# Performance work log

Measured on AMD Instinct MI355X. Metric: run time of the kernel, lower is better.

## Reference

```python
import jax, jax.numpy as jnp
import numpy as np

S, B, C = 56, 32, 1024
T = 48
H = 1024          # hidden_size_decoder (== context_size C)
EMB = 512
RANK = 128
VOCAB = 32000


def setup_inputs() -> dict:
    key = jax.random.key(0)
    ks = jax.random.split(key, 16)
    w = 0.05
    inp = {
        "encoded": jax.random.normal(ks[0], (S, B, C), jnp.float32),
        "encoder_state": jax.random.normal(ks[1], (2, B, H), jnp.float32) * 0.1,
        "tgt_tokens": jax.random.randint(ks[2], (B, T), 0, VOCAB),
        "enc_lens": jax.random.randint(ks[3], (B,), S // 2, S + 1).astype(jnp.int32),
        "tgt_lens": jax.random.randint(ks[4], (B,), T // 2, T + 1).astype(jnp.int32),
        "E": jax.random.normal(ks[5], (VOCAB, RANK), jnp.float32) * w,
        "P": jax.random.normal(ks[6], (RANK, EMB), jnp.float32) * w,
        "W0": jax.random.normal(ks[7], (EMB + C, 4 * H), jnp.float32) * w,
        "U0": jax.random.normal(ks[8], (H, 4 * H), jnp.float32) * w,
        "b0": jnp.zeros((4 * H,), jnp.float32),
        "W1": jax.random.normal(ks[9], (H, 4 * H), jnp.float32) * w,
        "U1": jax.random.normal(ks[10], (H, 4 * H), jnp.float32) * w,
        "b1": jnp.zeros((4 * H,), jnp.float32),
        "Wo": jax.random.normal(ks[11], (H + C, EMB), jnp.float32) * w,
        "bo": jnp.zeros((EMB,), jnp.float32),
    }
    return inp


def _lstm_cell(x, h, c, W, U, b):
    gates = x @ W + h @ U + b                      # [B, 4H]
    i, f, g, o = jnp.split(gates, 4, axis=-1)      # torch LSTMCell gate order
    c_new = jax.nn.sigmoid(f) * c + jax.nn.sigmoid(i) * jnp.tanh(g)
    h_new = jax.nn.sigmoid(o) * jnp.tanh(c_new)
    return h_new, c_new


def reference(encoded, encoder_state, tgt_tokens, enc_lens, tgt_lens,
              E, P, W0, U0, b0, W1, U1, b1, Wo, bo):
    # encoded: [S, B, C] (padded encoder outputs), encoder_state: [L=2, B, H]
    enc_b = jnp.transpose(encoded, (1, 0, 2))                 # [B, S, C]
    enc_mask = jnp.arange(S)[None, :] >= enc_lens[:, None]    # [B, S] True = pad

    # factorized embedding lookup (dropout p=0)
    emb = (E[tgt_tokens] @ P)                                 # [B, T, EMB]
    emb_t = jnp.transpose(emb, (1, 0, 2))[: T - 1]            # [T-1, B, EMB]

    h0 = encoder_state                                        # [2, B, H]
    c0 = jnp.zeros_like(encoder_state)
    ctx0 = jnp.zeros((B, C), encoded.dtype)

    def step(carry, x_emb):
        h, c, ctx = carry
        x = jnp.concatenate([x_emb, ctx], axis=-1)            # [B, EMB+C]
        h0n, c0n = _lstm_cell(x, h[0], c[0], W0, U0, b0)
        h1n, c1n = _lstm_cell(h0n, h[1], c[1], W1, U1, b1)
        query = h1n                                           # no context projection
        scores = jnp.einsum("bsc,bc->bs", enc_b, query)       # [B, S]
        scores = jnp.where(enc_mask, -jnp.inf, scores)
        p_att = jax.nn.softmax(scores, axis=-1)
        ctx_new = jnp.einsum("bs,bsc->bc", p_att, enc_b)      # [B, C]
        return (jnp.stack([h0n, h1n]), jnp.stack([c0n, c1n]), ctx_new), (h1n, ctx_new)

    _, (decs, ctxs) = jax.lax.scan(step, (h0, c0, ctx0), emb_t)  # each [T-1, B, *]

    feats = jnp.concatenate([decs, ctxs], axis=-1)            # [T-1, B, H+C]
    hproj = jnp.tanh(feats @ Wo + bo)                          # [T-1, B, EMB]
    logits = (hproj @ P.T) @ E.T                               # [T-1, B, VOCAB]

    labels = tgt_tokens[:, 1:].T                               # [T-1, B]
    logp = jax.nn.log_softmax(logits, axis=-1)
    nll = -jnp.take_along_axis(logp, labels[..., None], axis=-1)[..., 0]
    valid = jnp.arange(T - 1)[:, None] < (tgt_lens[None, :] - 1)  # step t predicts token t+1
    loss = jnp.sum(jnp.where(valid, nll, 0.0))                 # CrossEntropyLoss(reduction='sum')
    return loss
```

## Files before the change

### kernel.cpp

```cpp
#include <hip/hip_runtime.h>
#include <math.h>

#define S_   56
#define B_   32
#define C_   1024
#define T_   48
#define TS   47
#define H_   1024
#define EMB_ 512
#define RANK_ 128
#define VOCAB_ 32000
#define G4   4096
#define NBLK 256

#define FL_DONE 8192
#define FL_P    8224
#define FL_SIZE 10496

using bf16x8 = __attribute__((ext_vector_type(8))) __bf16;
using f32x4  = __attribute__((ext_vector_type(4))) float;

__device__ __forceinline__ float sigmoidf_(float x){ return 1.0f/(1.0f+expf(-x)); }
__device__ __forceinline__ float b2f(__bf16 x){ return (float)x; }
__device__ __forceinline__ f32x4 z4(){ f32x4 z = {0.f,0.f,0.f,0.f}; return z; }

#define AG __HIP_MEMORY_SCOPE_AGENT
__device__ __forceinline__ void stc_u64(void* p, unsigned long long v){
  __hip_atomic_store((unsigned long long*)p, v, __ATOMIC_RELAXED, AG);
}

struct RedShared {
  float red[4][2][16][18];
};
struct AttnShared {
  union { float hS[1024]; float cred[7][64][8]; } u;
  float sS[64];
  float pS[64];
};
union alignas(16) SharedU { RedShared r; AttnShared a; };

__device__ __forceinline__ void bar_arrive(unsigned* bars, int bi, unsigned e){
  asm volatile("s_waitcnt vmcnt(0)" ::: "memory");
  __syncthreads();
  if (threadIdx.x == 0)
    __hip_atomic_store(bars + (size_t)bi*32, e, __ATOMIC_RELAXED, AG);
}
__device__ __forceinline__ void bar_wait_all(unsigned* bars, int bi, unsigned e){
  if (bi == 255){
    if (threadIdx.x < 256){
      while (__hip_atomic_load(bars + (size_t)threadIdx.x*32, __ATOMIC_RELAXED, AG) < e) {}
    }
    __syncthreads();
    if (threadIdx.x == 0)
      __hip_atomic_store(bars + FL_DONE, e, __ATOMIC_RELAXED, AG);
  } else {
    if (threadIdx.x == 0){
      while (__hip_atomic_load(bars + FL_DONE, __ATOMIC_RELAXED, AG) < e) {}
    }
    __syncthreads();
  }
  asm volatile("" ::: "memory");
}
__device__ __forceinline__ void bar_wait_direct(unsigned* bars, unsigned e){
  if (threadIdx.x < 256){
    while (__hip_atomic_load(bars + (size_t)threadIdx.x*32, __ATOMIC_RELAXED, AG) < e) {}
  }
  __syncthreads();
  asm volatile("" ::: "memory");
}
__device__ __forceinline__ void pflag_wait(unsigned* bars, unsigned t){
  if (threadIdx.x < 64){
    while (__hip_atomic_load(bars + FL_P + (size_t)threadIdx.x*32, __ATOMIC_RELAXED, AG) < t)
      __builtin_amdgcn_s_sleep(2);
  }
  __syncthreads();
  asm volatile("" ::: "memory");
}

__global__ void k_init(const float* __restrict__ es, __bf16* h0bm1, __bf16* fm1,
                       unsigned* bars){
  int i = blockIdx.x*blockDim.x + threadIdx.x;
  if (i < 32*H_){
    int b = i >> 10, j = i & 1023;
    h0bm1[(size_t)b*1024 + j]       = (__bf16)es[i];
    fm1[(size_t)b*2048 + j]         = (__bf16)es[32*H_ + i];
    fm1[(size_t)b*2048 + 1024 + j]  = (__bf16)0.0f;
  }
  if (i < FL_SIZE) bars[i] = 0u;
}

__global__ void k_cvt(const float* __restrict__ src, __bf16* __restrict__ dst, int n){
  int i = (blockIdx.x*blockDim.x + threadIdx.x)*4;
  if (i < n){
    float4 v = *(const float4*)(src + i);
    dst[i+0]=(__bf16)v.x; dst[i+1]=(__bf16)v.y; dst[i+2]=(__bf16)v.z; dst[i+3]=(__bf16)v.w;
  }
}

__global__ void k_embed(const float* __restrict__ E, const float* __restrict__ P,
                        const int* __restrict__ tok, __bf16* __restrict__ embb){
  int blk = blockIdx.x;
  int t = blk >> 5, b = blk & 31, tid = threadIdx.x;
  __shared__ float er[RANK_];
  int tk = tok[b*T_ + t];
  er[tid] = E[(size_t)tk*RANK_ + tid];
  __syncthreads();
  float4 acc = {0.f,0.f,0.f,0.f};
  int e = tid*4;
  for (int r2 = 0; r2 < RANK_; r2++){
    float ev = er[r2];
    float4 p = *(const float4*)(P + (size_t)r2*EMB_ + e);
    acc.x += ev*p.x; acc.y += ev*p.y; acc.z += ev*p.z; acc.w += ev*p.w;
  }
  size_t o = (size_t)blk*EMB_ + e;
  embb[o+0]=(__bf16)acc.x; embb[o+1]=(__bf16)acc.y;
  embb[o+2]=(__bf16)acc.z; embb[o+3]=(__bf16)acc.w;
}

__global__ void k_pack2(const float* __restrict__ W, int K1, const float* __restrict__ U,
                        __bf16* __restrict__ dst, int NCH){
  int ch = blockIdx.x;
  int g  = blockIdx.y >> 2;
  int band = blockIdx.y & 3;
  int tid = threadIdx.x;
  __shared__ __bf16 Tl[32][264];
  {
    int r = tid>>3, cs = tid&7;
    int kk = ch*32 + r;
    const float* src = (kk < K1) ? (W + (size_t)kk*G4 + g*1024 + band*256 + cs*32)
                                 : (U + (size_t)(kk-K1)*G4 + g*1024 + band*256 + cs*32);
    #pragma unroll
    for (int u=0;u<8;u++){
      float4 v = *(const float4*)(src + u*4);
      Tl[r][cs*32+u*4+0]=(__bf16)v.x; Tl[r][cs*32+u*4+1]=(__bf16)v.y;
      Tl[r][cs*32+u*4+2]=(__bf16)v.z; Tl[r][cs*32+u*4+3]=(__bf16)v.w;
    }
  }
  __syncthreads();
  int bil = tid>>2, aq = tid&3;
  int bi = band*64 + bil;
  #pragma unroll
  for (int q=0;q<4;q++){
    __bf16 o8[8];
    #pragma unroll
    for (int i=0;i<8;i++) o8[i] = Tl[aq*8+i][bil*4+q];
    int lane = aq*16 + g*4 + q;
    *(bf16x8*)(dst + (((size_t)bi*NCH + ch)*64 + lane)*8) = *(bf16x8*)o8;
  }
}

__global__ void k_packB(const float* __restrict__ src, __bf16* __restrict__ dst,
                        int K, int N, int tr){
  int kk0 = blockIdx.x*32, j0 = blockIdx.y*16, lane = threadIdx.x;
  int am = lane&15, aq = lane>>4;
  int j = j0 + am;
  __bf16 o8[8];
  #pragma unroll
  for (int i=0;i<8;i++){
    int k = kk0 + aq*8 + i;
    float v = tr ? src[(size_t)j*K + k] : src[(size_t)k*N + j];
    o8[i] = (__bf16)v;
  }
  int NCH = K/32, jt = j0>>4, ch = kk0>>5;
  *(bf16x8*)(dst + (((size_t)jt*NCH + ch)*64 + lane)*8) = *(bf16x8*)o8;
}

template<int NC>
__device__ __forceinline__ void accum(f32x4& acc0, f32x4& acc1,
    const __bf16* __restrict__ abase, int rs, const __bf16* wlds,
    int ch0, int am, int aq, int lane)
{
  const __bf16* a0p = abase + (size_t)am*rs + aq*8;
  const __bf16* a1p = abase + (size_t)(am+16)*rs + aq*8;
  const __bf16* wl  = wlds + (size_t)lane*8;
  #pragma unroll
  for (int c=0;c<NC;c++){
    int ch = ch0 + c;
    bf16x8 a0 = *(const bf16x8*)(a0p + (size_t)ch*32);
    bf16x8 a1 = *(const bf16x8*)(a1p + (size_t)ch*32);
    bf16x8 w  = *(const bf16x8*)(wl  + (size_t)ch*512);
    acc0 = __builtin_amdgcn_mfma_f32_16x16x32_bf16(a0, w, acc0, 0, 0, 0);
    acc1 = __builtin_amdgcn_mfma_f32_16x16x32_bf16(a1, w, acc1, 0, 0, 0);
  }
}

__device__ __forceinline__ void reduce_cell(SharedU& su, const f32x4& acc0, const f32x4& acc1,
    int bi, int tid, const float* __restrict__ bias, float& creg,
    __bf16* __restrict__ hout, int stride)
{
  int kw = tid>>6, lane = tid&63, am = lane&15, aq = lane>>4;
  if (kw >= 4){
    #pragma unroll
    for (int rg=0;rg<4;rg++){
      su.r.red[kw-4][0][aq*4+rg][am] = acc0[rg];
      su.r.red[kw-4][1][aq*4+rg][am] = acc1[rg];
    }
  }
  __syncthreads();
  if (kw < 4){
    #pragma unroll
    for (int rg=0;rg<4;rg++){
      su.r.red[kw][0][aq*4+rg][am] += acc0[rg];
      su.r.red[kw][1][aq*4+rg][am] += acc1[rg];
    }
  }
  __syncthreads();
  if (tid < 128){
    int b = tid>>2, q = tid&3;
    int mt = b>>4, r = b&15;
    float G0=0.f, G1=0.f, G2=0.f, G3=0.f;
    #pragma unroll
    for (int w2=0; w2<4; w2++){
      G0 += su.r.red[w2][mt][r][q];
      G1 += su.r.red[w2][mt][r][4+q];
      G2 += su.r.red[w2][mt][r][8+q];
      G3 += su.r.red[w2][mt][r][12+q];
    }
    int j = bi*4 + q;
    float gi = G0 + bias[j];
    float gf = G1 + bias[1024 + j];
    float gg = G2 + bias[2048 + j];
    float go = G3 + bias[3072 + j];
    float ii = sigmoidf_(gi), ff = sigmoidf_(gf), gv = tanhf(gg), oo = sigmoidf_(go);
    float cv = ff*creg + ii*gv;
    float hv = oo*tanhf(cv);
    creg = cv;
    union { __bf16 h; unsigned short s; } hu; hu.h = (__bf16)hv;
    unsigned h0v = hu.s;
    unsigned h1v = __shfl_down(h0v, 1);
    unsigned h2v = __shfl_down(h0v, 2);
    unsigned h3v = __shfl_down(h0v, 3);
    if (q == 0){
      unsigned long long pk = (unsigned long long)(h0v & 0xffffu)
                            | ((unsigned long long)(h1v & 0xffffu) << 16)
                            | ((unsigned long long)(h2v & 0xffffu) << 32)
                            | ((unsigned long long)(h3v & 0xffffu) << 48);
      stc_u64(hout + (size_t)b*stride + bi*4, pk);
    }
  }
}

__device__ __forceinline__ void attn_block(AttnShared& sa, int b, int chalf, int tid,
    const __bf16* __restrict__ encb, const int* __restrict__ enc_lens,
    __bf16* __restrict__ fbt)
{
  if (tid < 128){
    bf16x8 h8 = *(const bf16x8*)(fbt + (size_t)b*2048 + tid*8);
    #pragma unroll
    for (int u=0;u<8;u++) sa.u.hS[tid*8+u] = b2f(h8[u]);
  }
  __syncthreads();
  int w = tid >> 6, lane = tid & 63;
  for (int s = w; s < S_; s += 8){
    const __bf16* er = encb + ((size_t)s*32 + b)*C_;
    float a = 0.f;
    #pragma unroll
    for (int half = 0; half < 2; half++){
      int k = lane*8 + half*512;
      bf16x8 e8 = *(const bf16x8*)(er + k);
      #pragma unroll
      for (int u=0;u<8;u++) a += b2f(e8[u]) * sa.u.hS[k+u];
    }
    #pragma unroll
    for (int off=32; off>0; off>>=1) a += __shfl_down(a, off);
    if (lane == 0) sa.sS[s] = a;
  }
  __syncthreads();
  if (tid < 64){
    int len = enc_lens[b];
    float sc = (tid < len && tid < S_) ? sa.sS[tid] : -1e30f;
    float m = sc;
    #pragma unroll
    for (int off=32; off>0; off>>=1) m = fmaxf(m, __shfl_xor(m, off));
    float e = expf(sc - m);
    float ssum = e;
    #pragma unroll
    for (int off=32; off>0; off>>=1) ssum += __shfl_xor(ssum, off);
    sa.pS[tid] = e / ssum;
  }
  __syncthreads();
  int cg = tid & 63, sg = tid >> 6;
  float a8[8];
  #pragma unroll
  for (int i=0;i<8;i++) a8[i] = 0.f;
  for (int s = sg; s < S_; s += 8){
    float p = sa.pS[s];
    bf16x8 e8 = *(const bf16x8*)(encb + ((size_t)s*32 + b)*C_ + chalf*512 + cg*8);
    #pragma unroll
    for (int i=0;i<8;i++) a8[i] += p * b2f(e8[i]);
  }
  if (sg > 0){
    #pragma unroll
    for (int i=0;i<8;i++) sa.u.cred[sg-1][cg][i] = a8[i];
  }
  __syncthreads();
  if (sg == 0){
    union { __bf16 bb[8]; unsigned long long u[2]; } cu;
    #pragma unroll
    for (int i=0;i<8;i++){
      float v = a8[i];
      #pragma unroll
      for (int k=0;k<7;k++) v += sa.u.cred[k][cg][i];
      cu.bb[i] = (__bf16)v;
    }
    stc_u64(fbt + (size_t)b*2048 + 1024 + chalf*512 + cg*8,     cu.u[0]);
    stc_u64(fbt + (size_t)b*2048 + 1024 + chalf*512 + cg*8 + 4, cu.u[1]);
  }
}

__global__ __launch_bounds__(512) void k_loop(
    const __bf16* __restrict__ WP0, const __bf16* __restrict__ WP1,
    const float* __restrict__ b0, const float* __restrict__ b1,
    __bf16* __restrict__ h0b,
    __bf16* __restrict__ featsb,
    const __bf16* __restrict__ embb,
    const __bf16* __restrict__ encb, const int* __restrict__ enc_lens,
    unsigned* bars)
{
  __shared__ __bf16 wB0[80*512];
  __shared__ __bf16 wB1[64*512];
  __shared__ SharedU su;
  int bi = blockIdx.x, tid = threadIdx.x;
  int kw = tid>>6, lane = tid&63, am = lane&15, aq = lane>>4;

  {
    const bf16x8* g0 = (const bf16x8*)(WP0 + (size_t)bi*80*512);
    const bf16x8* g1 = (const bf16x8*)(WP1 + (size_t)bi*64*512);
    bf16x8* l0 = (bf16x8*)wB0;
    bf16x8* l1 = (bf16x8*)wB1;
    for (int idx = tid; idx < 80*64; idx += 512) l0[idx] = g0[idx];
    for (int idx = tid; idx < 64*64; idx += 512) l1[idx] = g1[idx];
  }
  __syncthreads();

  float c0r = 0.f, c1r = 0.f;
  f32x4 g00 = z4(), g01 = z4(), g10 = z4(), g11 = z4();

  accum<2>(g00, g01, embb,                 512,  wB0, kw*2,    am, aq, lane);
  accum<4>(g00, g01, h0b - 32768 - 1536,   1024, wB0, 48+kw*4, am, aq, lane);

  unsigned e = 0;
  for (int t = 0; t < TS; t++){
    const __bf16* fprev = featsb + ((size_t)(t-1))*65536;
    __bf16* h0t = h0b + (size_t)t*32768;
    __bf16* ft  = featsb + (size_t)t*65536;

    pflag_wait(bars, (unsigned)t);
    accum<4>(g00, g01, fprev + 512, 2048, wB0, 16+kw*4, am, aq, lane);
    reduce_cell(su, g00, g01, bi, tid, b0, c0r, h0t, 1024);
    g00 = z4(); g01 = z4();
    bar_arrive(bars, bi, ++e);
    accum<4>(g10, g11, fprev - 1024, 2048, wB1, 32+kw*4, am, aq, lane);
    bar_wait_all(bars, bi, e);

    accum<4>(g10, g11, h0t, 1024, wB1, kw*4, am, aq, lane);
    reduce_cell(su, g10, g11, bi, tid, b1, c1r, ft, 2048);
    g10 = z4(); g11 = z4();
    bar_arrive(bars, bi, ++e);
    if (t + 1 < TS){
      accum<2>(g00, g01, embb + (size_t)(t+1)*16384, 512,  wB0, kw*2,    am, aq, lane);
      accum<4>(g00, g01, h0t - 1536,                 1024, wB0, 48+kw*4, am, aq, lane);
    }

    if (bi < 64){
      bar_wait_direct(bars, e);
      attn_block(su.a, bi & 31, bi >> 5, tid, encb, enc_lens, ft);
      asm volatile("s_waitcnt vmcnt(0)" ::: "memory");
      __syncthreads();
      if (tid == 0)
        __hip_atomic_store(bars + FL_P + (size_t)bi*32, (unsigned)(t+1), __ATOMIC_RELAXED, AG);
    }
  }
}

__global__ __launch_bounds__(256) void k_hproj_mfma(
    const __bf16* __restrict__ fb, const __bf16* __restrict__ WoP,
    const float* __restrict__ bo, __bf16* __restrict__ hpb)
{
  int nt = blockIdx.x, jb = blockIdx.y, tid = threadIdx.x;
  int w = tid>>6, lane = tid&63;
  int mt = w&1, jw = w>>1;
  int am = lane&15, aq = lane>>4;
  const __bf16* aRow = fb + ((size_t)(nt*32 + mt*16 + am))*2048 + aq*8;
  int jt = jb*2 + jw;
  const __bf16* bptr = WoP + ((size_t)jt*64)*512 + lane*8;
  f32x4 acc = {0,0,0,0};
  bf16x8 ar0 = *(const bf16x8*)(aRow);
  bf16x8 br0 = *(const bf16x8*)(bptr);
  bf16x8 ar1 = *(const bf16x8*)(aRow + 32);
  bf16x8 br1 = *(const bf16x8*)(bptr + 512);
  for (int ch = 0; ch < 64; ch += 2){
    bf16x8 a0 = ar0, b0 = br0, a1 = ar1, b1 = br1;
    if (ch + 2 < 64){
      ar0 = *(const bf16x8*)(aRow + (ch+2)*32);
      br0 = *(const bf16x8*)(bptr + (size_t)(ch+2)*512);
      ar1 = *(const bf16x8*)(aRow + (ch+3)*32);
      br1 = *(const bf16x8*)(bptr + (size_t)(ch+3)*512);
    }
    acc = __builtin_amdgcn_mfma_f32_16x16x32_bf16(a0, b0, acc, 0, 0, 0);
    acc = __builtin_amdgcn_mfma_f32_16x16x32_bf16(a1, b1, acc, 0, 0, 0);
  }
  int jcol = jb*32 + jw*16 + am;
  float bv = bo[jcol];
  #pragma unroll
  for (int rg=0; rg<4; rg++){
    int m = nt*32 + mt*16 + aq*4 + rg;
    hpb[(size_t)m*512 + jcol] = (__bf16)tanhf(acc[rg] + bv);
  }
}

__global__ __launch_bounds__(256) void k_rproj_mfma(
    const __bf16* __restrict__ hpb, const __bf16* __restrict__ PP,
    __bf16* __restrict__ rb)
{
  int nt = blockIdx.x, jb = blockIdx.y, tid = threadIdx.x;
  int w = tid>>6, lane = tid&63;
  int mt = w&1, jw = w>>1;
  int am = lane&15, aq = lane>>4;
  const __bf16* aRow = hpb + ((size_t)(nt*32 + mt*16 + am))*512 + aq*8;
  int jt = jb*2 + jw;
  const __bf16* bptr = PP + ((size_t)jt*16)*512 + lane*8;
  f32x4 acc = {0,0,0,0};
  #pragma unroll
  for (int ch = 0; ch < 16; ch++){
    bf16x8 a = *(const bf16x8*)(aRow + ch*32);
    bf16x8 b = *(const bf16x8*)(bptr + (size_t)ch*512);
    acc = __builtin_amdgcn_mfma_f32_16x16x32_bf16(a, b, acc, 0, 0, 0);
  }
  int jcol = jb*32 + jw*16 + am;
  #pragma unroll
  for (int rg=0; rg<4; rg++){
    int m = nt*32 + mt*16 + aq*4 + rg;
    rb[(size_t)m*RANK_ + jcol] = (__bf16)acc[rg];
  }
}

__global__ __launch_bounds__(256) void k_vocab2(
    const __bf16* __restrict__ rb, const __bf16* __restrict__ Eb,
    const int* __restrict__ tok,
    float* __restrict__ mpart, float* __restrict__ lpart,
    float* __restrict__ lablog)
{
  int vc = blockIdx.x, tid = threadIdx.x;
  int w = tid>>6, lane = tid&63;
  int am = lane&15, aq = lane>>4;
  int vb = vc*128 + w*32;
  bf16x8 bfr[2][4];
  #pragma unroll
  for (int vt=0; vt<2; vt++)
    #pragma unroll
    for (int ks=0; ks<4; ks++)
      bfr[vt][ks] = *(const bf16x8*)(Eb + ((size_t)(vb + vt*16 + am))*RANK_ + ks*32 + aq*8);

  __shared__ float redM[4][32], redL[4][32];
  for (int nt = 0; nt < TS; nt++){
    f32x4 acc[2][2] = {{{0,0,0,0},{0,0,0,0}},{{0,0,0,0},{0,0,0,0}}};
    #pragma unroll
    for (int mt=0; mt<2; mt++){
      #pragma unroll
      for (int ks=0; ks<4; ks++){
        bf16x8 a = *(const bf16x8*)(rb + ((size_t)(nt*32 + mt*16 + am))*RANK_ + ks*32 + aq*8);
        acc[mt][0] = __builtin_amdgcn_mfma_f32_16x16x32_bf16(a, bfr[0][ks], acc[mt][0], 0,0,0);
        acc[mt][1] = __builtin_amdgcn_mfma_f32_16x16x32_bf16(a, bfr[1][ks], acc[mt][1], 0,0,0);
      }
    }
    #pragma unroll
    for (int mt=0; mt<2; mt++){
      #pragma unroll
      for (int rg=0; rg<4; rg++){
        int row = mt*16 + aq*4 + rg;
        int n = nt*32 + row;
        int lbl = tok[row*T_ + nt + 1];
        float v0 = acc[mt][0][rg], v1 = acc[mt][1][rg];
        if (vb + am == lbl)      lablog[n] = v0;
        if (vb + 16 + am == lbl) lablog[n] = v1;
        float m = fmaxf(v0, v1);
        #pragma unroll
        for (int off=1; off<16; off<<=1) m = fmaxf(m, __shfl_xor(m, off));
        float l = expf(v0 - m) + expf(v1 - m);
        #pragma unroll
        for (int off=1; off<16; off<<=1) l += __shfl_xor(l, off);
        if (am == 0){ redM[w][row] = m; redL[w][row] = l; }
      }
    }
    __syncthreads();
    if (tid < 32){
      float M = fmaxf(fmaxf(redM[0][tid], redM[1][tid]), fmaxf(redM[2][tid], redM[3][tid]));
      float L = 0.f;
      #pragma unroll
      for (int ww=0; ww<4; ww++) L += redL[ww][tid]*expf(redM[ww][tid] - M);
      mpart[(size_t)(nt*32 + tid)*250 + vc] = M;
      lpart[(size_t)(nt*32 + tid)*250 + vc] = L;
    }
    __syncthreads();
  }
}

__global__ void k_loss1(const float* __restrict__ mpart, const float* __restrict__ lpart,
                        const float* __restrict__ lablog, const int* __restrict__ tgt_lens,
                        float* __restrict__ tpart){
  int t = blockIdx.x, tid = threadIdx.x;
  int row = tid >> 3, cq = tid & 7;
  int n = t*32 + row;
  float m = -1e30f;
  for (int c = cq; c < 250; c += 8) m = fmaxf(m, mpart[(size_t)n*250 + c]);
  #pragma unroll
  for (int off=1; off<8; off<<=1) m = fmaxf(m, __shfl_xor(m, off));
  float l = 0.f;
  for (int c = cq; c < 250; c += 8) l += lpart[(size_t)n*250 + c]*expf(mpart[(size_t)n*250 + c] - m);
  #pragma unroll
  for (int off=1; off<8; off<<=1) l += __shfl_xor(l, off);
  __shared__ float red[32];
  if (cq == 0)
    red[row] = (t < tgt_lens[row] - 1) ? (m + logf(l) - lablog[n]) : 0.f;
  __syncthreads();
  if (tid == 0){
    float s = 0.f;
    #pragma unroll
    for (int i=0;i<32;i++) s += red[i];
    tpart[t] = s;
  }
}

__global__ void k_loss2(const float* __restrict__ tpart, float* __restrict__ out){
  int tid = threadIdx.x;
  float v = (tid < TS) ? tpart[tid] : 0.f;
  #pragma unroll
  for (int off=32; off>0; off>>=1) v += __shfl_down(v, off);
  if (tid == 0) out[0] = v;
}

extern "C" void kernel_launch(void* const* d_in, const int* in_sizes, int n_in,
                              void* d_out, int out_size, void* d_ws, size_t ws_size,
                              hipStream_t stream){
  const float* enc      = (const float*)d_in[0];
  const float* es       = (const float*)d_in[1];
  const int*   tok      = (const int*)  d_in[2];
  const int*   enc_lens = (const int*)  d_in[3];
  const int*   tgt_lens = (const int*)  d_in[4];
  const float* E        = (const float*)d_in[5];
  const float* P        = (const float*)d_in[6];
  const float* W0       = (const float*)d_in[7];
  const float* U0       = (const float*)d_in[8];
  const float* b0       = (const float*)d_in[9];
  const float* W1       = (const float*)d_in[10];
  const float* U1       = (const float*)d_in[11];
  const float* b1       = (const float*)d_in[12];
  const float* Wo       = (const float*)d_in[13];
  const float* bo       = (const float*)d_in[14];
  float* out = (float*)d_out;

  float* fb = (float*)d_ws;
  size_t fo = 0;
  float* mpart = fb + fo; fo += (size_t)TS*32*250;
  float* lpart = fb + fo; fo += (size_t)TS*32*250;
  float* lab   = fb + fo; fo += (size_t)TS*32;
  float* tpart = fb + fo; fo += 64;
  unsigned* bars = (unsigned*)(fb + fo); fo += FL_SIZE;
  __bf16* bb = (__bf16*)(fb + fo);
  size_t bo2 = 0;
  __bf16* WP0    = bb + bo2; bo2 += (size_t)4096*2560;
  __bf16* WP1    = bb + bo2; bo2 += (size_t)4096*2048;
  __bf16* encb   = bb + bo2; bo2 += (size_t)S_*32*C_;
  __bf16* embb   = bb + bo2; bo2 += (size_t)TS*32*EMB_;
  __bf16* rbuf   = bb + bo2; bo2 += (size_t)TS*32*RANK_;
  __bf16* WoP    = bb + bo2; bo2 += (size_t)2048*512;
  __bf16* PP     = bb + bo2; bo2 += (size_t)512*128;
  __bf16* featsb0= bb + bo2; bo2 += (size_t)(TS+1)*32*2048;
  __bf16* hpb    = bb + bo2; bo2 += (size_t)TS*32*EMB_;
  __bf16* h0b0   = bb + bo2; bo2 += (size_t)(TS+1)*32*1024;
  __bf16* Eb     = WP0;

  __bf16* featsb = featsb0 + (size_t)32*2048;
  __bf16* h0b    = h0b0 + (size_t)32*1024;

  k_init<<<128, 256, 0, stream>>>(es, h0b0, featsb0, bars);
  k_cvt<<<(S_*32*C_/4 + 255)/256, 256, 0, stream>>>(enc, encb, S_*32*C_);
  k_embed<<<TS*32, 128, 0, stream>>>(E, P, tok, embb);
  k_pack2<<<dim3(80,16), 256, 0, stream>>>(W0, 1536, U0, WP0, 80);
  k_pack2<<<dim3(64,16), 256, 0, stream>>>(W1, 1024, U1, WP1, 64);
  k_packB<<<dim3(64,32), 64, 0, stream>>>(Wo, WoP, 2048, 512, 0);
  k_packB<<<dim3(16,8), 64, 0, stream>>>(P, PP, 512, 128, 1);

  k_loop<<<NBLK, 512, 0, stream>>>(WP0, WP1, b0, b1, h0b, featsb,
                                   embb, encb, enc_lens, bars);

  k_cvt<<<(VOCAB_*RANK_/4 + 255)/256, 256, 0, stream>>>(E, Eb, VOCAB_*RANK_);

  k_hproj_mfma<<<dim3(TS,16), 256, 0, stream>>>(featsb, WoP, bo, hpb);
  k_rproj_mfma<<<dim3(TS,4), 256, 0, stream>>>(hpb, PP, rbuf);
  k_vocab2<<<250, 256, 0, stream>>>(rbuf, Eb, tok, mpart, lpart, lab);
  k_loss1<<<TS, 256, 0, stream>>>(mpart, lpart, lab, tgt_lens, tpart);
  k_loss2<<<1, 64, 0, stream>>>(tpart, out);
}
```

Baseline: 1.392 ms.

## Pack LSTM weights inside persistent loop, merge prep kernels, flatten grid barrier

The separate weight-packing kernels and their global bf16 staging buffers are removed. Each persistent block now loads its fp32 W/U columns directly and converts and scatters them into shared memory itself. The encoder conversion is merged into the init kernel, and the E conversion moves ahead of the loop so Eb gets its own buffer. The two-level barrier through a single done-flag is replaced by every block polling all 256 arrival flags with a short sleep, and the attention flag wait sleeps less. This saves launches and a global round trip but adds strided fp32 loads at loop start and more polling traffic on the barrier.

```diff
diff --git a/kernel.cpp b/kernel.cpp
--- a/kernel.cpp
+++ b/kernel.cpp
@@ -13,7 +13,6 @@
 #define G4   4096
 #define NBLK 256
 
-#define FL_DONE 8192
 #define FL_P    8224
 #define FL_SIZE 10496
 
@@ -45,25 +44,10 @@
   if (threadIdx.x == 0)
     __hip_atomic_store(bars + (size_t)bi*32, e, __ATOMIC_RELAXED, AG);
 }
-__device__ __forceinline__ void bar_wait_all(unsigned* bars, int bi, unsigned e){
-  if (bi == 255){
-    if (threadIdx.x < 256){
-      while (__hip_atomic_load(bars + (size_t)threadIdx.x*32, __ATOMIC_RELAXED, AG) < e) {}
-    }
-    __syncthreads();
-    if (threadIdx.x == 0)
-      __hip_atomic_store(bars + FL_DONE, e, __ATOMIC_RELAXED, AG);
-  } else {
-    if (threadIdx.x == 0){
-      while (__hip_atomic_load(bars + FL_DONE, __ATOMIC_RELAXED, AG) < e) {}
-    }
-    __syncthreads();
-  }
-  asm volatile("" ::: "memory");
-}
-__device__ __forceinline__ void bar_wait_direct(unsigned* bars, unsigned e){
+__device__ __forceinline__ void bar_wait(unsigned* bars, unsigned e){
   if (threadIdx.x < 256){
-    while (__hip_atomic_load(bars + (size_t)threadIdx.x*32, __ATOMIC_RELAXED, AG) < e) {}
+    while (__hip_atomic_load(bars + (size_t)threadIdx.x*32, __ATOMIC_RELAXED, AG) < e)
+      __builtin_amdgcn_s_sleep(1);
   }
   __syncthreads();
   asm volatile("" ::: "memory");
@@ -71,15 +55,22 @@
 __device__ __forceinline__ void pflag_wait(unsigned* bars, unsigned t){
   if (threadIdx.x < 64){
     while (__hip_atomic_load(bars + FL_P + (size_t)threadIdx.x*32, __ATOMIC_RELAXED, AG) < t)
-      __builtin_amdgcn_s_sleep(2);
+      __builtin_amdgcn_s_sleep(1);
   }
   __syncthreads();
   asm volatile("" ::: "memory");
 }
 
-__global__ void k_init(const float* __restrict__ es, __bf16* h0bm1, __bf16* fm1,
+__global__ void k_prep(const float* __restrict__ enc, __bf16* __restrict__ encb,
+                       const float* __restrict__ es, __bf16* h0bm1, __bf16* fm1,
                        unsigned* bars){
   int i = blockIdx.x*blockDim.x + threadIdx.x;
+  int i4 = i*4;
+  if (i4 < S_*32*C_){
+    float4 v = *(const float4*)(enc + i4);
+    encb[i4+0]=(__bf16)v.x; encb[i4+1]=(__bf16)v.y;
+    encb[i4+2]=(__bf16)v.z; encb[i4+3]=(__bf16)v.w;
+  }
   if (i < 32*H_){
     int b = i >> 10, j = i & 1023;
     h0bm1[(size_t)b*1024 + j]       = (__bf16)es[i];
@@ -115,38 +106,6 @@
   size_t o = (size_t)blk*EMB_ + e;
   embb[o+0]=(__bf16)acc.x; embb[o+1]=(__bf16)acc.y;
   embb[o+2]=(__bf16)acc.z; embb[o+3]=(__bf16)acc.w;
-}
-
-__global__ void k_pack2(const float* __restrict__ W, int K1, const float* __restrict__ U,
-                        __bf16* __restrict__ dst, int NCH){
-  int ch = blockIdx.x;
-  int g  = blockIdx.y >> 2;
-  int band = blockIdx.y & 3;
-  int tid = threadIdx.x;
-  __shared__ __bf16 Tl[32][264];
-  {
-    int r = tid>>3, cs = tid&7;
-    int kk = ch*32 + r;
-    const float* src = (kk < K1) ? (W + (size_t)kk*G4 + g*1024 + band*256 + cs*32)
-                                 : (U + (size_t)(kk-K1)*G4 + g*1024 + band*256 + cs*32);
-    #pragma unroll
-    for (int u=0;u<8;u++){
-      float4 v = *(const float4*)(src + u*4);
-      Tl[r][cs*32+u*4+0]=(__bf16)v.x; Tl[r][cs*32+u*4+1]=(__bf16)v.y;
-      Tl[r][cs*32+u*4+2]=(__bf16)v.z; Tl[r][cs*32+u*4+3]=(__bf16)v.w;
-    }
-  }
-  __syncthreads();
-  int bil = tid>>2, aq = tid&3;
-  int bi = band*64 + bil;
-  #pragma unroll
-  for (int q=0;q<4;q++){
-    __bf16 o8[8];
-    #pragma unroll
-    for (int i=0;i<8;i++) o8[i] = Tl[aq*8+i][bil*4+q];
-    int lane = aq*16 + g*4 + q;
-    *(bf16x8*)(dst + (((size_t)bi*NCH + ch)*64 + lane)*8) = *(bf16x8*)o8;
-  }
 }
 
 __global__ void k_packB(const float* __restrict__ src, __bf16* __restrict__ dst,
@@ -309,7 +268,8 @@
 }
 
 __global__ __launch_bounds__(512) void k_loop(
-    const __bf16* __restrict__ WP0, const __bf16* __restrict__ WP1,
+    const float* __restrict__ W0, const float* __restrict__ U0,
+    const float* __restrict__ W1, const float* __restrict__ U1,
     const float* __restrict__ b0, const float* __restrict__ b1,
     __bf16* __restrict__ h0b,
     __bf16* __restrict__ featsb,
@@ -323,13 +283,21 @@
   int bi = blockIdx.x, tid = threadIdx.x;
   int kw = tid>>6, lane = tid&63, am = lane&15, aq = lane>>4;
 
-  {
-    const bf16x8* g0 = (const bf16x8*)(WP0 + (size_t)bi*80*512);
-    const bf16x8* g1 = (const bf16x8*)(WP1 + (size_t)bi*64*512);
-    bf16x8* l0 = (bf16x8*)wB0;
-    bf16x8* l1 = (bf16x8*)wB1;
-    for (int idx = tid; idx < 80*64; idx += 512) l0[idx] = g0[idx];
-    for (int idx = tid; idx < 64*64; idx += 512) l1[idx] = g1[idx];
+  for (int idx = tid; idx < 2560*4; idx += 512){
+    int kk = idx >> 2, g = idx & 3;
+    const float* src = (kk < 1536) ? (W0 + (size_t)kk*G4) : (U0 + (size_t)(kk-1536)*G4);
+    float4 v = *(const float4*)(src + g*1024 + bi*4);
+    int ch = kk >> 5, r5 = kk & 31, aq2 = r5 >> 3, i8 = r5 & 7;
+    __bf16* d = wB0 + ch*512 + (aq2*16 + g*4)*8 + i8;
+    d[0] = (__bf16)v.x; d[8] = (__bf16)v.y; d[16] = (__bf16)v.z; d[24] = (__bf16)v.w;
+  }
+  for (int idx = tid; idx < 2048*4; idx += 512){
+    int kk = idx >> 2, g = idx & 3;
+    const float* src = (kk < 1024) ? (W1 + (size_t)kk*G4) : (U1 + (size_t)(kk-1024)*G4);
+    float4 v = *(const float4*)(src + g*1024 + bi*4);
+    int ch = kk >> 5, r5 = kk & 31, aq2 = r5 >> 3, i8 = r5 & 7;
+    __bf16* d = wB1 + ch*512 + (aq2*16 + g*4)*8 + i8;
+    d[0] = (__bf16)v.x; d[8] = (__bf16)v.y; d[16] = (__bf16)v.z; d[24] = (__bf16)v.w;
   }
   __syncthreads();
 
@@ -351,7 +319,7 @@
     g00 = z4(); g01 = z4();
     bar_arrive(bars, bi, ++e);
     accum<4>(g10, g11, fprev - 1024, 2048, wB1, 32+kw*4, am, aq, lane);
-    bar_wait_all(bars, bi, e);
+    bar_wait(bars, e);
 
     accum<4>(g10, g11, h0t, 1024, wB1, kw*4, am, aq, lane);
     reduce_cell(su, g10, g11, bi, tid, b1, c1r, ft, 2048);
@@ -363,7 +331,7 @@
     }
 
     if (bi < 64){
-      bar_wait_direct(bars, e);
+      bar_wait(bars, e);
       attn_block(su.a, bi & 31, bi >> 5, tid, encb, enc_lens, ft);
       asm volatile("s_waitcnt vmcnt(0)" ::: "memory");
       __syncthreads();
@@ -559,8 +527,6 @@
   unsigned* bars = (unsigned*)(fb + fo); fo += FL_SIZE;
   __bf16* bb = (__bf16*)(fb + fo);
   size_t bo2 = 0;
-  __bf16* WP0    = bb + bo2; bo2 += (size_t)4096*2560;
-  __bf16* WP1    = bb + bo2; bo2 += (size_t)4096*2048;
   __bf16* encb   = bb + bo2; bo2 += (size_t)S_*32*C_;
   __bf16* embb   = bb + bo2; bo2 += (size_t)TS*32*EMB_;
   __bf16* rbuf   = bb + bo2; bo2 += (size_t)TS*32*RANK_;
@@ -569,23 +535,19 @@
   __bf16* featsb0= bb + bo2; bo2 += (size_t)(TS+1)*32*2048;
   __bf16* hpb    = bb + bo2; bo2 += (size_t)TS*32*EMB_;
   __bf16* h0b0   = bb + bo2; bo2 += (size_t)(TS+1)*32*1024;
-  __bf16* Eb     = WP0;
+  __bf16* Eb     = bb + bo2; bo2 += (size_t)VOCAB_*RANK_;
 
   __bf16* featsb = featsb0 + (size_t)32*2048;
   __bf16* h0b    = h0b0 + (size_t)32*1024;
 
-  k_init<<<128, 256, 0, stream>>>(es, h0b0, featsb0, bars);
-  k_cvt<<<(S_*32*C_/4 + 255)/256, 256, 0, stream>>>(enc, encb, S_*32*C_);
+  k_prep<<<1792, 256, 0, stream>>>(enc, encb, es, h0b0, featsb0, bars);
   k_embed<<<TS*32, 128, 0, stream>>>(E, P, tok, embb);
-  k_pack2<<<dim3(80,16), 256, 0, stream>>>(W0, 1536, U0, WP0, 80);
-  k_pack2<<<dim3(64,16), 256, 0, stream>>>(W1, 1024, U1, WP1, 64);
   k_packB<<<dim3(64,32), 64, 0, stream>>>(Wo, WoP, 2048, 512, 0);
   k_packB<<<dim3(16,8), 64, 0, stream>>>(P, PP, 512, 128, 1);
-
-  k_loop<<<NBLK, 512, 0, stream>>>(WP0, WP1, b0, b1, h0b, featsb,
+  k_cvt<<<(VOCAB_*RANK_/4 + 255)/256, 256, 0, stream>>>(E, Eb, VOCAB_*RANK_);
+
+  k_loop<<<NBLK, 512, 0, stream>>>(W0, U0, W1, U1, b0, b1, h0b, featsb,
                                    embb, encb, enc_lens, bars);
-
-  k_cvt<<<(VOCAB_*RANK_/4 + 255)/256, 256, 0, stream>>>(E, Eb, VOCAB_*RANK_);
 
   k_hproj_mfma<<<dim3(TS,16), 256, 0, stream>>>(featsb, WoP, bo, hpb);
   k_rproj_mfma<<<dim3(TS,4), 256, 0, stream>>>(hpb, PP, rbuf);
```

New measurement: 1.400 ms. No clear change (+0.6%).
